# Kernel tuning notes

Measured on AMD Instinct MI355X. Metric: run time of the kernel, lower is better.

## Reference

```python
import jax, jax.numpy as jnp
import numpy as np

B, S, H = 2, 2048, 2048
NH, NKV, HD = 16, 4, 128
THETA = 10000.0


def _rope_cos_sin(seq_len, head_dim, theta, dtype):
    inv_freq = 1.0 / (theta ** (jnp.arange(0, head_dim, 2, dtype=jnp.float32) / head_dim))
    t = jnp.arange(seq_len, dtype=jnp.float32)
    freqs = t[:, None] * inv_freq[None, :]          # [S, HD/2]
    emb = jnp.concatenate([freqs, freqs], axis=-1)  # [S, HD]
    return jnp.cos(emb).astype(dtype), jnp.sin(emb).astype(dtype)


def _rotate_half(x):
    d = x.shape[-1] // 2
    return jnp.concatenate([-x[..., d:], x[..., :d]], axis=-1)


def setup_inputs() -> dict:
    key = jax.random.key(0)
    ks = jax.random.split(key, 5)
    x = jax.random.normal(ks[0], (B, S, H), dtype=jnp.float32)
    Wq = jax.random.normal(ks[1], (NH * HD, H), dtype=jnp.float32) * 0.02
    Wk = jax.random.normal(ks[2], (NKV * HD, H), dtype=jnp.float32) * 0.02
    Wv = jax.random.normal(ks[3], (NKV * HD, H), dtype=jnp.float32) * 0.02
    Wo = jax.random.normal(ks[4], (H, H), dtype=jnp.float32) * 0.02
    causal = jnp.tril(jnp.ones((S, S), dtype=bool))
    attention_mask = jnp.where(causal, 0.0, -1e9).astype(jnp.float32)[None, None]  # [1,1,S,S]
    return {"x": x, "attention_mask": attention_mask, "Wq": Wq, "Wk": Wk, "Wv": Wv, "Wo": Wo}


def reference(x, attention_mask, Wq, Wk, Wv, Wo):
    b, s, _ = x.shape
    q = (x @ Wq.T).reshape(b, s, NH, HD).transpose(0, 2, 1, 3)    # [b,nh,s,hd]
    k = (x @ Wk.T).reshape(b, s, NKV, HD).transpose(0, 2, 1, 3)   # [b,nkv,s,hd]
    v = (x @ Wv.T).reshape(b, s, NKV, HD).transpose(0, 2, 1, 3)
    cos, sin = _rope_cos_sin(s, HD, THETA, x.dtype)               # [s,hd] each
    cos = cos[None, None]; sin = sin[None, None]
    q = q * cos + _rotate_half(q) * sin
    k = k * cos + _rotate_half(k) * sin
    rep = NH // NKV
    k = jnp.repeat(k, rep, axis=1)                                 # [b,nh,s,hd]
    v = jnp.repeat(v, rep, axis=1)
    scores = jnp.einsum('bhqd,bhkd->bhqk', q, k) / jnp.sqrt(jnp.asarray(HD, x.dtype))
    scores = scores + attention_mask
    attn = jax.nn.softmax(scores, axis=-1)
    out = jnp.einsum('bhqk,bhkd->bhqd', attn, v)                   # [b,nh,s,hd]
    out = out.transpose(0, 2, 1, 3).reshape(b, s, NH * HD)
    return out @ Wo.T
```

## Files before the change

kernel.cpp:

```cpp
#include <hip/hip_runtime.h>

typedef unsigned short u16;
typedef __bf16 bf16x8 __attribute__((ext_vector_type(8)));
typedef float f32x4 __attribute__((ext_vector_type(4)));
typedef short s16x4 __attribute__((ext_vector_type(4)));

#define S_LEN  2048
#define NHEADS 16
#define NKVH   4
#define HDIM   128
#define BB     2
#define MROWS  4096
#define QKV_N  3072
#define HID    2048

__device__ __forceinline__ u16 f2b(float f) {
  union { float f; unsigned u; } x; x.f = f;
  unsigned r = x.u + 0x7fffu + ((x.u >> 16) & 1u);
  return (u16)(r >> 16);
}
__device__ __forceinline__ float b2f(u16 v) {
  union { unsigned u; float f; } x; x.u = ((unsigned)v) << 16;
  return x.f;
}
__device__ __forceinline__ void gload_lds16(const u16* g, u16* l) {
  __builtin_amdgcn_global_load_lds((__attribute__((address_space(1))) void*)g,
                                   (__attribute__((address_space(3))) void*)l,
                                   16, 0, 0);
}
__device__ __forceinline__ unsigned cvtpk(float lo, float hi) {
  unsigned r;
  asm("v_cvt_pk_bf16_f32 %0, %1, %2" : "=v"(r) : "v"(lo), "v"(hi));
  return r;
}
#if __has_builtin(__builtin_amdgcn_mfma_f32_16x16x16bf16_1k)
__device__ __forceinline__ f32x4 mfma16(s16x4 a, s16x4 b, f32x4 c) {
  return __builtin_amdgcn_mfma_f32_16x16x16bf16_1k(a, b, c, 0, 0, 0);
}
#else
__device__ __forceinline__ f32x4 mfma16(s16x4 a, s16x4 b, f32x4 c) {
  asm("v_mfma_f32_16x16x16_bf16 %0, %1, %2, %0" : "+v"(c) : "v"(a), "v"(b));
  return c;
}
#endif

#define SBAR() do { __builtin_amdgcn_sched_barrier(0); \
                    __builtin_amdgcn_s_barrier();      \
                    __builtin_amdgcn_sched_barrier(0); } while (0)

#define PB_X   8192
#define PB_WQ  (PB_X + 4096)
#define PB_WK  (PB_WQ + 1024)
#define PB_WV  (PB_WK + 1024)
#define PB_WO  (PB_WV + 4096)
#define PB_CS  (PB_WO + 512)
__global__ void k_prep(const float* __restrict__ x,
                       const float* __restrict__ Wq, const float* __restrict__ Wk,
                       const float* __restrict__ Wv, const float* __restrict__ Wo,
                       u16* __restrict__ xb, u16* __restrict__ Wqkvb,
                       u16* __restrict__ Wob, float* __restrict__ cs)
{
  const int bid = blockIdx.x, tid = threadIdx.x;
  const float* src; u16* dst; int i;
  if (bid < PB_X)       { i = bid * 256 + tid;            src = x;  dst = xb; }
  else if (bid < PB_WQ) { i = (bid - PB_X) * 256 + tid;   src = Wq; dst = Wqkvb; }
  else if (bid < PB_WK) { i = (bid - PB_WQ) * 256 + tid;  src = Wk; dst = Wqkvb + (size_t)2048 * HID; }
  else if (bid < PB_WV) { i = (bid - PB_WK) * 256 + tid;  src = Wv; dst = Wqkvb + (size_t)2560 * HID; }
  else if (bid < PB_WO) { i = (bid - PB_WV) * 256 + tid;  src = Wo; dst = Wob; }
  else {
    const int p = (bid - PB_WO) * 256 + tid;
    const int s = p >> 6, j = p & 63;
    float inv = expf(-(float)j * 0.14391156831212787f);
    float ang = (float)s * inv;
    float c, sn; sincosf(ang, &sn, &c);
    cs[p * 2 + 0] = c; cs[p * 2 + 1] = sn;
    return;
  }
  float4 v = ((const float4*)src)[i];
  ushort4 o;
  o.x = f2b(v.x); o.y = f2b(v.y); o.z = f2b(v.z); o.w = f2b(v.w);
  ((ushort4*)dst)[i] = o;
}

#define MFMA_GRP(AV, BV, MO, NO)                                              \
  __builtin_amdgcn_s_setprio(1);                                              \
  _Pragma("unroll") for (int kk = 0; kk < 2; ++kk)                            \
  _Pragma("unroll") for (int mm = 0; mm < 4; ++mm)                            \
  _Pragma("unroll") for (int nn = 0; nn < 2; ++nn)                            \
    acc[(MO) + mm][(NO) + nn] = __builtin_amdgcn_mfma_f32_16x16x32_bf16(      \
        AV[kk][mm], BV[kk][nn], acc[(MO) + mm][(NO) + nn], 0, 0, 0);          \
  __builtin_amdgcn_s_setprio(0);

template <int OUT_BF16>
__global__ __launch_bounds__(512, 2) void k_gemm256(
    const u16* __restrict__ A, const u16* __restrict__ Bm, void* __restrict__ Cv,
    int M, int N, int K)
{
  __shared__ u16 AL[2][2][8192];
  __shared__ u16 BL[2][2][8192];
  const int tid = threadIdx.x;
  const int wave = tid >> 6, lane = tid & 63;
  const int l15 = lane & 15, l4 = lane >> 4;
  const int wr = wave >> 2, wc = wave & 3;
  const int gx = gridDim.x;
  const int nwg = gx * gridDim.y;
  int bid = blockIdx.y * gx + blockIdx.x;
  bid = (bid & 7) * (nwg >> 3) + (bid >> 3);
  const int col0 = (bid % gx) * 256, row0 = (bid / gx) * 256;

  int srcOff[2], dstD[2];
#pragma unroll
  for (int li = 0; li < 2; ++li) {
    const int D = (li * 512 + tid) * 16;
    const int off_p = D & 1023, si = D >> 10;
    const int off_l = off_p ^ (((off_p >> 9) & 1) << 5);
    const int R = si >> 1, C = si & 1;
    const int row = R * 16 + (off_l >> 6);
    const int colb = C * 64 + (off_l & 63);
    srcOff[li] = row * K + (colb >> 1);
    dstD[li] = D;
  }
  const int laneoff = (l15 * 64 + l4 * 16) ^ ((l15 >> 3) << 5);

  auto stage = [&](const u16* __restrict__ G, int grow0, int kb, u16* lds) {
#pragma unroll
    for (int li = 0; li < 2; ++li)
      gload_lds16(G + (size_t)grow0 * K + kb + srcOff[li],
                  (u16*)((char*)lds + dstD[li]));
  };

  f32x4 acc[8][4];
#pragma unroll
  for (int m = 0; m < 8; ++m)
#pragma unroll
    for (int n = 0; n < 4; ++n) acc[m][n] = f32x4{0.f, 0.f, 0.f, 0.f};

  const int nk = K >> 6;
  stage(A,  row0,       0,  &AL[0][0][0]);
  stage(A,  row0 + 128, 0,  &AL[0][1][0]);
  stage(Bm, col0,       0,  &BL[0][0][0]);
  stage(Bm, col0 + 128, 0,  &BL[0][1][0]);
  stage(A,  row0,       64, &AL[1][0][0]);
  stage(A,  row0 + 128, 64, &AL[1][1][0]);
  asm volatile("s_waitcnt vmcnt(4)" ::: "memory");
  SBAR();

  for (int t = 0; t < nk; ++t) {
    const int bi = t & 1;
    const bool sB = (t + 1 < nk);
    const bool sA = (t + 2 < nk);
    const char* Ab = (const char*)&AL[bi][wr][0];
    const char* Bb = (const char*)&BL[bi][wc >> 1][0] + (wc & 1) * 8192;
    bf16x8 a0[2][4], a1[2][4], b0[2][2], b1[2][2];
#pragma unroll
    for (int kk = 0; kk < 2; ++kk)
#pragma unroll
      for (int m = 0; m < 4; ++m)
        a0[kk][m] = *(const bf16x8*)(Ab + m * 2048 + kk * 1024 + laneoff);
#pragma unroll
    for (int kk = 0; kk < 2; ++kk)
#pragma unroll
      for (int n = 0; n < 2; ++n)
        b0[kk][n] = *(const bf16x8*)(Bb + n * 2048 + kk * 1024 + laneoff);
    if (sB) stage(Bm, col0, (t + 1) * 64, &BL[bi ^ 1][0][0]);
    SBAR();
    MFMA_GRP(a0, b0, 0, 0);
    SBAR();
#pragma unroll
    for (int kk = 0; kk < 2; ++kk)
#pragma unroll
      for (int m = 0; m < 4; ++m)
        a1[kk][m] = *(const bf16x8*)(Ab + (m + 4) * 2048 + kk * 1024 + laneoff);
    if (sB) stage(Bm, col0 + 128, (t + 1) * 64, &BL[bi ^ 1][1][0]);
    SBAR();
    MFMA_GRP(a1, b0, 4, 0);
    SBAR();
#pragma unroll
    for (int kk = 0; kk < 2; ++kk)
#pragma unroll
      for (int n = 0; n < 2; ++n)
        b1[kk][n] = *(const bf16x8*)(Bb + (n + 2) * 2048 + kk * 1024 + laneoff);
    if (sA) stage(A, row0, (t + 2) * 64, &AL[bi][0][0]);
    SBAR();
    MFMA_GRP(a1, b1, 4, 2);
    SBAR();
    if (sA) {
      stage(A, row0 + 128, (t + 2) * 64, &AL[bi][1][0]);
      asm volatile("s_waitcnt vmcnt(4)" ::: "memory");
    } else if (sB) {
      asm volatile("s_waitcnt vmcnt(0)" ::: "memory");
    }
    SBAR();
    MFMA_GRP(a0, b1, 0, 2);
    SBAR();
  }

#pragma unroll
  for (int m = 0; m < 8; ++m) {
    const int r = row0 + wr * 128 + m * 16 + l4 * 4;
#pragma unroll
    for (int n = 0; n < 4; ++n) {
      const int c = col0 + wc * 64 + n * 16 + l15;
#pragma unroll
      for (int j = 0; j < 4; ++j) {
        const float v = acc[m][n][j];
        if (OUT_BF16) ((u16*)Cv)[(size_t)(r + j) * N + c] = f2b(v);
        else          ((float*)Cv)[(size_t)(r + j) * N + c] = v;
      }
    }
  }
}

template <int OUT_BF16>
__global__ __launch_bounds__(256) void k_gemm_bt(
    const u16* __restrict__ A, const u16* __restrict__ Bm, void* __restrict__ Cv,
    int M, int N, int K)
{
  __shared__ u16 Al[2][128 * 32];
  __shared__ u16 Bl[2][128 * 32];
  const int tid = threadIdx.x;
  const int wave = tid >> 6, lane = tid & 63;
  const int l15 = lane & 15, l4 = lane >> 4;
  const int wr = wave >> 1, wc = wave & 1;
  const int row0 = blockIdx.y * 128, col0 = blockIdx.x * 128;

  f32x4 zero = {0.f, 0.f, 0.f, 0.f};
  f32x4 acc[4][4];
#pragma unroll
  for (int m = 0; m < 4; ++m)
#pragma unroll
    for (int n = 0; n < 4; ++n) acc[m][n] = zero;

  const int e0 = lane * 8;
  auto stage = [&](int buf, int kb) {
#pragma unroll
    for (int it = 0; it < 2; ++it) {
      const int chunk = it * 4 + wave;
      const int e = chunk * 512 + e0;
      const int r = e >> 5, c = e & 31;
      gload_lds16(A + (size_t)(row0 + r) * K + kb + c, &Al[buf][chunk * 512]);
      gload_lds16(Bm + (size_t)(col0 + r) * K + kb + c, &Bl[buf][chunk * 512]);
    }
  };

  stage(0, 0);
  asm volatile("s_waitcnt vmcnt(0)" ::: "memory");
  SBAR();
  int cur = 0;
  for (int kb = 0; kb < K; kb += 32) {
    if (kb + 32 < K) stage(cur ^ 1, kb + 32);
    bf16x8 af[4], bfv[4];
#pragma unroll
    for (int m = 0; m < 4; ++m)
      af[m] = *(const bf16x8*)(&Al[cur][(wr * 64 + m * 16 + l15) * 32 + l4 * 8]);
#pragma unroll
    for (int n = 0; n < 4; ++n)
      bfv[n] = *(const bf16x8*)(&Bl[cur][(wc * 64 + n * 16 + l15) * 32 + l4 * 8]);
    __builtin_amdgcn_s_setprio(1);
#pragma unroll
    for (int m = 0; m < 4; ++m)
#pragma unroll
      for (int n = 0; n < 4; ++n)
        acc[m][n] = __builtin_amdgcn_mfma_f32_16x16x32_bf16(af[m], bfv[n], acc[m][n], 0, 0, 0);
    __builtin_amdgcn_s_setprio(0);
    asm volatile("s_waitcnt vmcnt(0)" ::: "memory");
    SBAR();
    cur ^= 1;
  }
#pragma unroll
  for (int m = 0; m < 4; ++m) {
    const int r = row0 + wr * 64 + m * 16 + l4 * 4;
#pragma unroll
    for (int n = 0; n < 4; ++n) {
      const int c = col0 + wc * 64 + n * 16 + l15;
#pragma unroll
      for (int j = 0; j < 4; ++j) {
        const float v = acc[m][n][j];
        if (OUT_BF16) ((u16*)Cv)[(size_t)(r + j) * N + c] = f2b(v);
        else          ((float*)Cv)[(size_t)(r + j) * N + c] = v;
      }
    }
  }
}

__global__ __launch_bounds__(256) void k_ropev(
    const u16* __restrict__ qkv, const float* __restrict__ cs,
    u16* __restrict__ Qr, u16* __restrict__ Kr, u16* __restrict__ Vt)
{
  const int blk = blockIdx.x;
  const int b = blk >> 8, s0 = (blk & 255) << 3;
  const int tid = threadIdx.x;
  const float S2 = 0.08838834764831845f * 1.4426950408889634f;
#pragma unroll
  for (int p = tid; p < 1024; p += 256) {
    const int s = p >> 7, rem = p & 127, h = rem >> 3, j8 = (rem & 7) * 8;
    const int sg = s0 + s;
    const u16* src = qkv + (size_t)(b * S_LEN + sg) * QKV_N + h * 128 + j8;
    union { uint4 v; u16 u[8]; } lo, hi, olo, ohi;
    lo.v = *(const uint4*)(src);
    hi.v = *(const uint4*)(src + 64);
    const float* cp = cs + (size_t)(sg * 64 + j8) * 2;
#pragma unroll
    for (int k = 0; k < 8; ++k) {
      const float c = cp[k * 2], sn = cp[k * 2 + 1];
      const float x0 = b2f(lo.u[k]), x1 = b2f(hi.u[k]);
      olo.u[k] = f2b((x0 * c - x1 * sn) * S2);
      ohi.u[k] = f2b((x1 * c + x0 * sn) * S2);
    }
    u16* dst = Qr + ((size_t)(b * NHEADS + h) * S_LEN + sg) * HDIM + j8;
    *(uint4*)(dst) = olo.v;
    *(uint4*)(dst + 64) = ohi.v;
  }
  {
    const int p = tid;
    const int s = p >> 5, rem = p & 31, h = rem >> 3, j8 = (rem & 7) * 8;
    const int sg = s0 + s;
    const u16* src = qkv + (size_t)(b * S_LEN + sg) * QKV_N + 2048 + h * 128 + j8;
    union { uint4 v; u16 u[8]; } lo, hi, olo, ohi;
    lo.v = *(const uint4*)(src);
    hi.v = *(const uint4*)(src + 64);
    const float* cp = cs + (size_t)(sg * 64 + j8) * 2;
#pragma unroll
    for (int k = 0; k < 8; ++k) {
      const float c = cp[k * 2], sn = cp[k * 2 + 1];
      const float x0 = b2f(lo.u[k]), x1 = b2f(hi.u[k]);
      olo.u[k] = f2b(x0 * c - x1 * sn);
      ohi.u[k] = f2b(x1 * c + x0 * sn);
    }
    u16* dst = Kr + ((size_t)(b * NKVH + h) * S_LEN + sg) * HDIM + j8;
    *(uint4*)(dst) = olo.v;
    *(uint4*)(dst + 64) = ohi.v;
  }
#pragma unroll
  for (int vi = 0; vi < 2; ++vi) {
    const int idx = vi * 256 + tid, h = idx >> 7, d = idx & 127;
    union { u16 u[8]; uint4 v; } bb;
#pragma unroll
    for (int s = 0; s < 8; ++s)
      bb.u[s] = qkv[(size_t)(b * S_LEN + s0 + s) * QKV_N + 2560 + idx];
    *(uint4*)(Vt + ((size_t)(b * NKVH + h) * HDIM + d) * S_LEN + s0) = bb.v;
  }
}

__device__ __forceinline__ void attn_qtile(
    int qt, int lastPhase,
    const u16* __restrict__ Q, const u16* __restrict__ Kg, const u16* __restrict__ Vg,
    u16* __restrict__ Out, int bh,
    u16* Kl0, u16* Kl1, u16* Vl0, u16* Vl1,
    const int (&ko)[4], const int (&vo)[4],
    int wave, int lane, int& cur)
{
  const int l15 = lane & 15, l4 = lane >> 4;
  const int b = bh >> 4, h = bh & 15;
  const int qw0 = qt * 64 + wave * 16;
  const u16* Qg = Q + ((size_t)bh * S_LEN + qw0) * HDIM;

  bf16x8 qf[4];
#pragma unroll
  for (int kc = 0; kc < 4; ++kc)
    qf[kc] = *(const bf16x8*)(Qg + l15 * HDIM + kc * 32 + l4 * 8);

  f32x4 zero = {0.f, 0.f, 0.f, 0.f};
  f32x4 oacc[8];
#pragma unroll
  for (int i = 0; i < 8; ++i) oacc[i] = zero;
  float m_r = -1e30f, l_p = 0.f;

  const int nt = qt + 1;
  const int qg = qw0 + l15;

  for (int t = 0; t < nt; ++t) {
    const int kt = t * 64;
    u16* Vb = cur ? Vl1 : Vl0;
#pragma unroll
    for (int it = 0; it < 4; ++it)
      gload_lds16(Vg + (size_t)vo[it] + kt, Vb + (it * 4 + wave) * 512);
    const int hasNext = (t + 1 < nt) || (!lastPhase);
    const int ktn = (t + 1 < nt) ? kt + 64 : 0;
    u16* Kn = cur ? Kl0 : Kl1;
    if (hasNext) {
#pragma unroll
      for (int it = 0; it < 4; ++it)
        gload_lds16(Kg + (size_t)ktn * HDIM + ko[it], Kn + (it * 4 + wave) * 512);
      asm volatile("s_waitcnt vmcnt(8)" ::: "memory");
    } else {
      asm volatile("s_waitcnt vmcnt(4)" ::: "memory");
    }
    __builtin_amdgcn_sched_barrier(0);
    __builtin_amdgcn_s_barrier();
    __builtin_amdgcn_sched_barrier(0);

    const char* Kb = (const char*)(cur ? Kl1 : Kl0);
    f32x4 s[4];
#pragma unroll
    for (int n = 0; n < 4; ++n) s[n] = zero;
    __builtin_amdgcn_s_setprio(1);
#pragma unroll
    for (int n = 0; n < 4; ++n) {
      const int row = n * 16 + l15;
#pragma unroll
      for (int kc = 0; kc < 4; ++kc) {
        const int ab = (row * 256 + kc * 64 + l4 * 16) ^ ((row & 7) << 4);
        bf16x8 kf = *(const bf16x8*)(Kb + ab);
        s[n] = __builtin_amdgcn_mfma_f32_16x16x32_bf16(kf, qf[kc], s[n], 0, 0, 0);
      }
    }
    __builtin_amdgcn_s_setprio(0);
    float sv[4][4];
    if (kt + 63 > qw0) {
#pragma unroll
      for (int n = 0; n < 4; ++n)
#pragma unroll
        for (int j = 0; j < 4; ++j) {
          float x = s[n][j];
          if (kt + n * 16 + l4 * 4 + j > qg) x = -1e30f;
          sv[n][j] = x;
        }
    } else {
#pragma unroll
      for (int n = 0; n < 4; ++n)
#pragma unroll
        for (int j = 0; j < 4; ++j) sv[n][j] = s[n][j];
    }
    float pm = sv[0][0];
#pragma unroll
    for (int n = 0; n < 4; ++n)
#pragma unroll
      for (int j = 0; j < 4; ++j) pm = fmaxf(pm, sv[n][j]);
    if (!__all(pm <= m_r + 11.5416f)) {
      float pf = fmaxf(pm, __shfl_xor(pm, 16, 64));
      pf = fmaxf(pf, __shfl_xor(pf, 32, 64));
      const float mn = fmaxf(m_r, pf);
      const float sc = exp2f(m_r - mn);
      m_r = mn;
      l_p *= sc;
      float scq[4];
#pragma unroll
      for (int j = 0; j < 4; ++j) scq[j] = __shfl(sc, l4 * 4 + j, 64);
#pragma unroll
      for (int nd = 0; nd < 8; ++nd)
#pragma unroll
        for (int j = 0; j < 4; ++j) oacc[nd][j] *= scq[j];
    }
    union { unsigned u[2]; s16x4 v; } a[4];
#pragma unroll
    for (int n = 0; n < 4; ++n) {
      const float p0 = exp2f(sv[n][0] - m_r);
      const float p1 = exp2f(sv[n][1] - m_r);
      const float p2 = exp2f(sv[n][2] - m_r);
      const float p3 = exp2f(sv[n][3] - m_r);
      l_p += (p0 + p1) + (p2 + p3);
      a[n].u[0] = cvtpk(p0, p1);
      a[n].u[1] = cvtpk(p2, p3);
    }
    if (hasNext) asm volatile("s_waitcnt vmcnt(4)" ::: "memory");
    else         asm volatile("s_waitcnt vmcnt(0)" ::: "memory");
    __builtin_amdgcn_sched_barrier(0);
    __builtin_amdgcn_s_barrier();
    __builtin_amdgcn_sched_barrier(0);
    __builtin_amdgcn_s_setprio(1);
#pragma unroll
    for (int nd = 0; nd < 8; ++nd) {
      const int d = nd * 16 + l15;
      const int rowb = d * 128, swz = (d & 7) << 4;
#pragma unroll
      for (int n = 0; n < 4; ++n) {
        const int ab = (rowb + n * 32 + l4 * 8) ^ swz;
        s16x4 vf = *(const s16x4*)((const char*)Vb + ab);
        oacc[nd] = mfma16(a[n].v, vf, oacc[nd]);
      }
    }
    __builtin_amdgcn_s_setprio(0);
    cur ^= 1;
  }

  l_p += __shfl_xor(l_p, 16, 64);
  l_p += __shfl_xor(l_p, 32, 64);
  float il[4];
#pragma unroll
  for (int j = 0; j < 4; ++j) il[j] = 1.f / __shfl(l_p, l4 * 4 + j, 64);
  const size_t obase = ((size_t)b * S_LEN + qw0 + l4 * 4) * HID + h * HDIM;
#pragma unroll
  for (int nd = 0; nd < 8; ++nd)
#pragma unroll
    for (int j = 0; j < 4; ++j)
      Out[obase + (size_t)j * HID + nd * 16 + l15] = f2b(oacc[nd][j] * il[j]);
}

__global__ __launch_bounds__(256) void k_attn(
    const u16* __restrict__ Q, const u16* __restrict__ Kr,
    const u16* __restrict__ Vt, u16* __restrict__ Out)
{
  __shared__ u16 Kl[2][64 * 128];
  __shared__ u16 Vl[2][128 * 64];
  const int tid = threadIdx.x;
  const int wave = tid >> 6, lane = tid & 63;
  const int bh = blockIdx.x;
  const int pairi = blockIdx.y;
  const int b = bh >> 4, h = bh & 15;
  const int kvh = h >> 2;

  const u16* Kg = Kr + (size_t)(b * NKVH + kvh) * S_LEN * HDIM;
  const u16* Vg = Vt + (size_t)(b * NKVH + kvh) * HDIM * S_LEN;

  int ko[4], vo[4];
#pragma unroll
  for (int it = 0; it < 4; ++it) {
    const int c = it * 4 + wave;
    const int L = c * 1024 + lane * 16;
    const int r = L >> 8;  const int w2 = (L & 255) ^ ((r & 7) << 4);
    ko[it] = r * HDIM + (w2 >> 1);
    const int d = L >> 7;  const int wv = (L & 127) ^ ((d & 7) << 4);
    vo[it] = d * S_LEN + (wv >> 1);
  }
#pragma unroll
  for (int it = 0; it < 4; ++it)
    gload_lds16(Kg + ko[it], &Kl[0][(it * 4 + wave) * 512]);

  int cur = 0;
  attn_qtile(31 - pairi, 0, Q, Kg, Vg, Out, bh, &Kl[0][0], &Kl[1][0],
             &Vl[0][0], &Vl[1][0], ko, vo, wave, lane, cur);
  attn_qtile(pairi,      1, Q, Kg, Vg, Out, bh, &Kl[0][0], &Kl[1][0],
             &Vl[0][0], &Vl[1][0], ko, vo, wave, lane, cur);
}

extern "C" void kernel_launch(void* const* d_in, const int* in_sizes, int n_in,
                              void* d_out, int out_size, void* d_ws, size_t ws_size,
                              hipStream_t stream)
{
  const float* x  = (const float*)d_in[0];
  const float* Wq = (const float*)d_in[2];
  const float* Wk = (const float*)d_in[3];
  const float* Wv = (const float*)d_in[4];
  const float* Wo = (const float*)d_in[5];
  float* out = (float*)d_out;

  u16* xb    = (u16*)d_ws;
  u16* Wqkvb = xb    + (size_t)MROWS * HID;
  u16* Wob   = Wqkvb + (size_t)QKV_N * HID;
  u16* qkv   = Wob   + (size_t)HID * HID;
  u16* Qr    = qkv   + (size_t)MROWS * QKV_N;
  u16* Kr    = Qr    + (size_t)BB * NHEADS * S_LEN * HDIM;
  u16* Vt    = Kr    + (size_t)BB * NKVH * S_LEN * HDIM;
  u16* attn  = Vt    + (size_t)BB * NKVH * S_LEN * HDIM;
  float* cs  = (float*)(attn + (size_t)MROWS * HID);

  k_prep<<<dim3(PB_CS), 256, 0, stream>>>(x, Wq, Wk, Wv, Wo, xb, Wqkvb, Wob, cs);
  k_gemm256<1><<<dim3(QKV_N / 256, MROWS / 256), 512, 0, stream>>>(xb, Wqkvb, qkv, MROWS, QKV_N, HID);
  k_ropev<<<dim3(BB * 256), 256, 0, stream>>>(qkv, cs, Qr, Kr, Vt);
  k_attn<<<dim3(BB * NHEADS, 16), 256, 0, stream>>>(Qr, Kr, Vt, attn);
  k_gemm_bt<0><<<dim3(HID / 128, MROWS / 128), 256, 0, stream>>>(attn, Wob, out, MROWS, HID, HID);
}
```

Baseline: 208.6 us.

## Split attention into one q-tile per block with 32-wide KV tiles; use 256 GEMM for output

The attention kernel now assigns one 64-row query tile to each block (32 blocks per head) instead of pairing two tiles per block. It steps over keys in 32-wide tiles with halved LDS buffers and a matching V swizzle layout. The output projection switches from the 128-tile GEMM to the existing 256-tile GEMM kernel. The aim is more parallelism and occupancy in attention and better reuse in the final GEMM, at the cost of more loop iterations, extra barriers and a less balanced causal workload across blocks.

```diff
diff --git a/kernel.cpp b/kernel.cpp
--- a/kernel.cpp
+++ b/kernel.cpp
@@ -211,78 +211,6 @@
   }
 }
 
-template <int OUT_BF16>
-__global__ __launch_bounds__(256) void k_gemm_bt(
-    const u16* __restrict__ A, const u16* __restrict__ Bm, void* __restrict__ Cv,
-    int M, int N, int K)
-{
-  __shared__ u16 Al[2][128 * 32];
-  __shared__ u16 Bl[2][128 * 32];
-  const int tid = threadIdx.x;
-  const int wave = tid >> 6, lane = tid & 63;
-  const int l15 = lane & 15, l4 = lane >> 4;
-  const int wr = wave >> 1, wc = wave & 1;
-  const int row0 = blockIdx.y * 128, col0 = blockIdx.x * 128;
-
-  f32x4 zero = {0.f, 0.f, 0.f, 0.f};
-  f32x4 acc[4][4];
-#pragma unroll
-  for (int m = 0; m < 4; ++m)
-#pragma unroll
-    for (int n = 0; n < 4; ++n) acc[m][n] = zero;
-
-  const int e0 = lane * 8;
-  auto stage = [&](int buf, int kb) {
-#pragma unroll
-    for (int it = 0; it < 2; ++it) {
-      const int chunk = it * 4 + wave;
-      const int e = chunk * 512 + e0;
-      const int r = e >> 5, c = e & 31;
-      gload_lds16(A + (size_t)(row0 + r) * K + kb + c, &Al[buf][chunk * 512]);
-      gload_lds16(Bm + (size_t)(col0 + r) * K + kb + c, &Bl[buf][chunk * 512]);
-    }
-  };
-
-  stage(0, 0);
-  asm volatile("s_waitcnt vmcnt(0)" ::: "memory");
-  SBAR();
-  int cur = 0;
-  for (int kb = 0; kb < K; kb += 32) {
-    if (kb + 32 < K) stage(cur ^ 1, kb + 32);
-    bf16x8 af[4], bfv[4];
-#pragma unroll
-    for (int m = 0; m < 4; ++m)
-      af[m] = *(const bf16x8*)(&Al[cur][(wr * 64 + m * 16 + l15) * 32 + l4 * 8]);
-#pragma unroll
-    for (int n = 0; n < 4; ++n)
-      bfv[n] = *(const bf16x8*)(&Bl[cur][(wc * 64 + n * 16 + l15) * 32 + l4 * 8]);
-    __builtin_amdgcn_s_setprio(1);
-#pragma unroll
-    for (int m = 0; m < 4; ++m)
-#pragma unroll
-      for (int n = 0; n < 4; ++n)
-        acc[m][n] = __builtin_amdgcn_mfma_f32_16x16x32_bf16(af[m], bfv[n], acc[m][n], 0, 0, 0);
-    __builtin_amdgcn_s_setprio(0);
-    asm volatile("s_waitcnt vmcnt(0)" ::: "memory");
-    SBAR();
-    cur ^= 1;
-  }
-#pragma unroll
-  for (int m = 0; m < 4; ++m) {
-    const int r = row0 + wr * 64 + m * 16 + l4 * 4;
-#pragma unroll
-    for (int n = 0; n < 4; ++n) {
-      const int c = col0 + wc * 64 + n * 16 + l15;
-#pragma unroll
-      for (int j = 0; j < 4; ++j) {
-        const float v = acc[m][n][j];
-        if (OUT_BF16) ((u16*)Cv)[(size_t)(r + j) * N + c] = f2b(v);
-        else          ((float*)Cv)[(size_t)(r + j) * N + c] = v;
-      }
-    }
-  }
-}
-
 __global__ __launch_bounds__(256) void k_ropev(
     const u16* __restrict__ qkv, const float* __restrict__ cs,
     u16* __restrict__ Qr, u16* __restrict__ Kr, u16* __restrict__ Vt)
@@ -342,18 +270,41 @@
   }
 }
 
-__device__ __forceinline__ void attn_qtile(
-    int qt, int lastPhase,
-    const u16* __restrict__ Q, const u16* __restrict__ Kg, const u16* __restrict__ Vg,
-    u16* __restrict__ Out, int bh,
-    u16* Kl0, u16* Kl1, u16* Vl0, u16* Vl1,
-    const int (&ko)[4], const int (&vo)[4],
-    int wave, int lane, int& cur)
+__global__ __launch_bounds__(256) void k_attn(
+    const u16* __restrict__ Q, const u16* __restrict__ Kr,
+    const u16* __restrict__ Vt, u16* __restrict__ Out)
 {
+  __shared__ u16 Kl[2][32 * 128];
+  __shared__ u16 Vl[2][64 * 64];
+  const int tid = threadIdx.x;
+  const int wave = tid >> 6, lane = tid & 63;
   const int l15 = lane & 15, l4 = lane >> 4;
+  const int bh = blockIdx.x;
+  const int by = blockIdx.y;
   const int b = bh >> 4, h = bh & 15;
+  const int kvh = h >> 2;
+  const int aa = by & 7, kk_ = by >> 3;
+  const int qt = (kk_ == 0) ? aa : (kk_ == 1) ? 15 - aa : (kk_ == 2) ? 16 + aa : 31 - aa;
+
+  const u16* Kg = Kr + (size_t)(b * NKVH + kvh) * S_LEN * HDIM;
+  const u16* Vg = Vt + (size_t)(b * NKVH + kvh) * HDIM * S_LEN;
+
+  int ko[2], vo[2];
+#pragma unroll
+  for (int it = 0; it < 2; ++it) {
+    const int c = it * 4 + wave;
+    const int L = c * 1024 + lane * 16;
+    const int r = L >> 8;
+    const int w2 = (L & 255) ^ ((r & 7) << 4);
+    ko[it] = r * HDIM + (w2 >> 1);
+    const int row = L >> 7;
+    const int wv = (L & 127) ^ ((row & 7) << 4);
+    const int d = row * 2 + (wv >> 6);
+    vo[it] = d * S_LEN + ((wv & 63) >> 1);
+  }
+
   const int qw0 = qt * 64 + wave * 16;
-  const u16* Qg = Q + ((size_t)bh * S_LEN + qw0) * HDIM;
+  const u16* Qg = Q + ((size_t)(b * NHEADS + h) * S_LEN + qw0) * HDIM;
 
   bf16x8 qf[4];
 #pragma unroll
@@ -366,37 +317,38 @@
   for (int i = 0; i < 8; ++i) oacc[i] = zero;
   float m_r = -1e30f, l_p = 0.f;
 
-  const int nt = qt + 1;
+  const int nt = 2 * qt + 2;
   const int qg = qw0 + l15;
+  int cur = 0;
+
+#pragma unroll
+  for (int it = 0; it < 2; ++it)
+    gload_lds16(Kg + ko[it], &Kl[0][(it * 4 + wave) * 512]);
 
   for (int t = 0; t < nt; ++t) {
-    const int kt = t * 64;
-    u16* Vb = cur ? Vl1 : Vl0;
-#pragma unroll
-    for (int it = 0; it < 4; ++it)
+    const int kt = t * 32;
+    u16* Vb = cur ? &Vl[1][0] : &Vl[0][0];
+#pragma unroll
+    for (int it = 0; it < 2; ++it)
       gload_lds16(Vg + (size_t)vo[it] + kt, Vb + (it * 4 + wave) * 512);
-    const int hasNext = (t + 1 < nt) || (!lastPhase);
-    const int ktn = (t + 1 < nt) ? kt + 64 : 0;
-    u16* Kn = cur ? Kl0 : Kl1;
+    const int hasNext = (t + 1 < nt);
     if (hasNext) {
-#pragma unroll
-      for (int it = 0; it < 4; ++it)
-        gload_lds16(Kg + (size_t)ktn * HDIM + ko[it], Kn + (it * 4 + wave) * 512);
-      asm volatile("s_waitcnt vmcnt(8)" ::: "memory");
+      u16* Kn = cur ? &Kl[0][0] : &Kl[1][0];
+#pragma unroll
+      for (int it = 0; it < 2; ++it)
+        gload_lds16(Kg + (size_t)(kt + 32) * HDIM + ko[it], Kn + (it * 4 + wave) * 512);
+      asm volatile("s_waitcnt vmcnt(4)" ::: "memory");
     } else {
-      asm volatile("s_waitcnt vmcnt(4)" ::: "memory");
-    }
-    __builtin_amdgcn_sched_barrier(0);
-    __builtin_amdgcn_s_barrier();
-    __builtin_amdgcn_sched_barrier(0);
-
-    const char* Kb = (const char*)(cur ? Kl1 : Kl0);
-    f32x4 s[4];
-#pragma unroll
-    for (int n = 0; n < 4; ++n) s[n] = zero;
+      asm volatile("s_waitcnt vmcnt(2)" ::: "memory");
+    }
+    SBAR();
+
+    const char* Kb = (const char*)(cur ? &Kl[1][0] : &Kl[0][0]);
+    f32x4 s[2];
+    s[0] = zero; s[1] = zero;
     __builtin_amdgcn_s_setprio(1);
 #pragma unroll
-    for (int n = 0; n < 4; ++n) {
+    for (int n = 0; n < 2; ++n) {
       const int row = n * 16 + l15;
 #pragma unroll
       for (int kc = 0; kc < 4; ++kc) {
@@ -406,27 +358,18 @@
       }
     }
     __builtin_amdgcn_s_setprio(0);
-    float sv[4][4];
-    if (kt + 63 > qw0) {
-#pragma unroll
-      for (int n = 0; n < 4; ++n)
-#pragma unroll
-        for (int j = 0; j < 4; ++j) {
-          float x = s[n][j];
-          if (kt + n * 16 + l4 * 4 + j > qg) x = -1e30f;
-          sv[n][j] = x;
-        }
-    } else {
-#pragma unroll
-      for (int n = 0; n < 4; ++n)
-#pragma unroll
-        for (int j = 0; j < 4; ++j) sv[n][j] = s[n][j];
-    }
-    float pm = sv[0][0];
-#pragma unroll
-    for (int n = 0; n < 4; ++n)
-#pragma unroll
-      for (int j = 0; j < 4; ++j) pm = fmaxf(pm, sv[n][j]);
+    if (kt + 31 > qw0) {
+#pragma unroll
+      for (int n = 0; n < 2; ++n)
+#pragma unroll
+        for (int j = 0; j < 4; ++j)
+          if (kt + n * 16 + l4 * 4 + j > qg) s[n][j] = -1e30f;
+    }
+    float pm = s[0][0];
+#pragma unroll
+    for (int n = 0; n < 2; ++n)
+#pragma unroll
+      for (int j = 0; j < 4; ++j) pm = fmaxf(pm, s[n][j]);
     if (!__all(pm <= m_r + 11.5416f)) {
       float pf = fmaxf(pm, __shfl_xor(pm, 16, 64));
       pf = fmaxf(pf, __shfl_xor(pf, 32, 64));
@@ -442,29 +385,28 @@
 #pragma unroll
         for (int j = 0; j < 4; ++j) oacc[nd][j] *= scq[j];
     }
-    union { unsigned u[2]; s16x4 v; } a[4];
-#pragma unroll
-    for (int n = 0; n < 4; ++n) {
-      const float p0 = exp2f(sv[n][0] - m_r);
-      const float p1 = exp2f(sv[n][1] - m_r);
-      const float p2 = exp2f(sv[n][2] - m_r);
-      const float p3 = exp2f(sv[n][3] - m_r);
+    union { unsigned u[2]; s16x4 v; } a[2];
+#pragma unroll
+    for (int n = 0; n < 2; ++n) {
+      const float p0 = exp2f(s[n][0] - m_r);
+      const float p1 = exp2f(s[n][1] - m_r);
+      const float p2 = exp2f(s[n][2] - m_r);
+      const float p3 = exp2f(s[n][3] - m_r);
       l_p += (p0 + p1) + (p2 + p3);
       a[n].u[0] = cvtpk(p0, p1);
       a[n].u[1] = cvtpk(p2, p3);
     }
-    if (hasNext) asm volatile("s_waitcnt vmcnt(4)" ::: "memory");
+    if (hasNext) asm volatile("s_waitcnt vmcnt(2)" ::: "memory");
     else         asm volatile("s_waitcnt vmcnt(0)" ::: "memory");
-    __builtin_amdgcn_sched_barrier(0);
-    __builtin_amdgcn_s_barrier();
-    __builtin_amdgcn_sched_barrier(0);
+    SBAR();
     __builtin_amdgcn_s_setprio(1);
 #pragma unroll
     for (int nd = 0; nd < 8; ++nd) {
       const int d = nd * 16 + l15;
-      const int rowb = d * 128, swz = (d & 7) << 4;
-#pragma unroll
-      for (int n = 0; n < 4; ++n) {
+      const int rowb = (d >> 1) * 128 + (d & 1) * 64;
+      const int swz = ((d >> 1) & 7) << 4;
+#pragma unroll
+      for (int n = 0; n < 2; ++n) {
         const int ab = (rowb + n * 32 + l4 * 8) ^ swz;
         s16x4 vf = *(const s16x4*)((const char*)Vb + ab);
         oacc[nd] = mfma16(a[n].v, vf, oacc[nd]);
@@ -485,43 +427,6 @@
 #pragma unroll
     for (int j = 0; j < 4; ++j)
       Out[obase + (size_t)j * HID + nd * 16 + l15] = f2b(oacc[nd][j] * il[j]);
-}
-
-__global__ __launch_bounds__(256) void k_attn(
-    const u16* __restrict__ Q, const u16* __restrict__ Kr,
-    const u16* __restrict__ Vt, u16* __restrict__ Out)
-{
-  __shared__ u16 Kl[2][64 * 128];
-  __shared__ u16 Vl[2][128 * 64];
-  const int tid = threadIdx.x;
-  const int wave = tid >> 6, lane = tid & 63;
-  const int bh = blockIdx.x;
-  const int pairi = blockIdx.y;
-  const int b = bh >> 4, h = bh & 15;
-  const int kvh = h >> 2;
-
-  const u16* Kg = Kr + (size_t)(b * NKVH + kvh) * S_LEN * HDIM;
-  const u16* Vg = Vt + (size_t)(b * NKVH + kvh) * HDIM * S_LEN;
-
-  int ko[4], vo[4];
-#pragma unroll
-  for (int it = 0; it < 4; ++it) {
-    const int c = it * 4 + wave;
-    const int L = c * 1024 + lane * 16;
-    const int r = L >> 8;  const int w2 = (L & 255) ^ ((r & 7) << 4);
-    ko[it] = r * HDIM + (w2 >> 1);
-    const int d = L >> 7;  const int wv = (L & 127) ^ ((d & 7) << 4);
-    vo[it] = d * S_LEN + (wv >> 1);
-  }
-#pragma unroll
-  for (int it = 0; it < 4; ++it)
-    gload_lds16(Kg + ko[it], &Kl[0][(it * 4 + wave) * 512]);
-
-  int cur = 0;
-  attn_qtile(31 - pairi, 0, Q, Kg, Vg, Out, bh, &Kl[0][0], &Kl[1][0],
-             &Vl[0][0], &Vl[1][0], ko, vo, wave, lane, cur);
-  attn_qtile(pairi,      1, Q, Kg, Vg, Out, bh, &Kl[0][0], &Kl[1][0],
-             &Vl[0][0], &Vl[1][0], ko, vo, wave, lane, cur);
 }
 
 extern "C" void kernel_launch(void* const* d_in, const int* in_sizes, int n_in,
@@ -548,6 +453,6 @@
   k_prep<<<dim3(PB_CS), 256, 0, stream>>>(x, Wq, Wk, Wv, Wo, xb, Wqkvb, Wob, cs);
   k_gemm256<1><<<dim3(QKV_N / 256, MROWS / 256), 512, 0, stream>>>(xb, Wqkvb, qkv, MROWS, QKV_N, HID);
   k_ropev<<<dim3(BB * 256), 256, 0, stream>>>(qkv, cs, Qr, Kr, Vt);
-  k_attn<<<dim3(BB * NHEADS, 16), 256, 0, stream>>>(Qr, Kr, Vt, attn);
-  k_gemm_bt<0><<<dim3(HID / 128, MROWS / 128), 256, 0, stream>>>(attn, Wob, out, MROWS, HID, HID);
-}
+  k_attn<<<dim3(BB * NHEADS, 32), 256, 0, stream>>>(Qr, Kr, Vt, attn);
+  k_gemm256<0><<<dim3(HID / 256, MROWS / 256), 512, 0, stream>>>(attn, Wob, out, MROWS, HID, HID);
+}
```

After: 226.9 us. 8.8% more time.

## Share K/V tiles across two GQA heads per attention block and swizzle GEMM blocks

Applied to the files above, without the earlier changes.

The attention kernel now runs 512 threads per block, with two query heads that share the same KV head, so each K/V tile staged in LDS serves twice as many waves. Each wave issues half as many global-to-LDS loads, and the grid shrinks from 32x16 to 16x16 blocks. The output-projection GEMM remaps block IDs into an XCD-aware order (bid&7 spreading) to improve L2 locality across chiplets. The cost is fewer, larger attention blocks, which may lower occupancy or load balance. The code also relies on an SBAR macro that is not defined in the shown portion.

```diff
diff --git a/kernel.cpp b/kernel.cpp
--- a/kernel.cpp
+++ b/kernel.cpp
@@ -222,7 +222,11 @@
   const int wave = tid >> 6, lane = tid & 63;
   const int l15 = lane & 15, l4 = lane >> 4;
   const int wr = wave >> 1, wc = wave & 1;
-  const int row0 = blockIdx.y * 128, col0 = blockIdx.x * 128;
+  const int gx = gridDim.x;
+  const int nwg = gx * gridDim.y;
+  int bid = blockIdx.y * gx + blockIdx.x;
+  bid = (bid & 7) * (nwg >> 3) + (bid >> 3);
+  const int row0 = (bid / gx) * 128, col0 = (bid % gx) * 128;
 
   f32x4 zero = {0.f, 0.f, 0.f, 0.f};
   f32x4 acc[4][4];
@@ -347,12 +351,12 @@
     const u16* __restrict__ Q, const u16* __restrict__ Kg, const u16* __restrict__ Vg,
     u16* __restrict__ Out, int bh,
     u16* Kl0, u16* Kl1, u16* Vl0, u16* Vl1,
-    const int (&ko)[4], const int (&vo)[4],
-    int wave, int lane, int& cur)
+    const int (&ko)[2], const int (&vo)[2],
+    int wave, int w4, int lane, int& cur)
 {
   const int l15 = lane & 15, l4 = lane >> 4;
   const int b = bh >> 4, h = bh & 15;
-  const int qw0 = qt * 64 + wave * 16;
+  const int qw0 = qt * 64 + w4 * 16;
   const u16* Qg = Q + ((size_t)bh * S_LEN + qw0) * HDIM;
 
   bf16x8 qf[4];
@@ -373,22 +377,20 @@
     const int kt = t * 64;
     u16* Vb = cur ? Vl1 : Vl0;
 #pragma unroll
-    for (int it = 0; it < 4; ++it)
-      gload_lds16(Vg + (size_t)vo[it] + kt, Vb + (it * 4 + wave) * 512);
+    for (int it = 0; it < 2; ++it)
+      gload_lds16(Vg + (size_t)vo[it] + kt, Vb + (it * 8 + wave) * 512);
     const int hasNext = (t + 1 < nt) || (!lastPhase);
     const int ktn = (t + 1 < nt) ? kt + 64 : 0;
     u16* Kn = cur ? Kl0 : Kl1;
     if (hasNext) {
 #pragma unroll
-      for (int it = 0; it < 4; ++it)
-        gload_lds16(Kg + (size_t)ktn * HDIM + ko[it], Kn + (it * 4 + wave) * 512);
-      asm volatile("s_waitcnt vmcnt(8)" ::: "memory");
+      for (int it = 0; it < 2; ++it)
+        gload_lds16(Kg + (size_t)ktn * HDIM + ko[it], Kn + (it * 8 + wave) * 512);
+      asm volatile("s_waitcnt vmcnt(4)" ::: "memory");
     } else {
-      asm volatile("s_waitcnt vmcnt(4)" ::: "memory");
-    }
-    __builtin_amdgcn_sched_barrier(0);
-    __builtin_amdgcn_s_barrier();
-    __builtin_amdgcn_sched_barrier(0);
+      asm volatile("s_waitcnt vmcnt(2)" ::: "memory");
+    }
+    SBAR();
 
     const char* Kb = (const char*)(cur ? Kl1 : Kl0);
     f32x4 s[4];
@@ -453,11 +455,9 @@
       a[n].u[0] = cvtpk(p0, p1);
       a[n].u[1] = cvtpk(p2, p3);
     }
-    if (hasNext) asm volatile("s_waitcnt vmcnt(4)" ::: "memory");
+    if (hasNext) asm volatile("s_waitcnt vmcnt(2)" ::: "memory");
     else         asm volatile("s_waitcnt vmcnt(0)" ::: "memory");
-    __builtin_amdgcn_sched_barrier(0);
-    __builtin_amdgcn_s_barrier();
-    __builtin_amdgcn_sched_barrier(0);
+    SBAR();
     __builtin_amdgcn_s_setprio(1);
 #pragma unroll
     for (int nd = 0; nd < 8; ++nd) {
@@ -487,7 +487,7 @@
       Out[obase + (size_t)j * HID + nd * 16 + l15] = f2b(oacc[nd][j] * il[j]);
 }
 
-__global__ __launch_bounds__(256) void k_attn(
+__global__ __launch_bounds__(512) void k_attn(
     const u16* __restrict__ Q, const u16* __restrict__ Kr,
     const u16* __restrict__ Vt, u16* __restrict__ Out)
 {
@@ -495,18 +495,20 @@
   __shared__ u16 Vl[2][128 * 64];
   const int tid = threadIdx.x;
   const int wave = tid >> 6, lane = tid & 63;
-  const int bh = blockIdx.x;
+  const int bx = blockIdx.x;
   const int pairi = blockIdx.y;
-  const int b = bh >> 4, h = bh & 15;
-  const int kvh = h >> 2;
+  const int kvh = bx & 3, b = (bx >> 2) & 1, hp = bx >> 3;
+  const int h = kvh * 4 + hp + (wave >> 2) * 2;
+  const int bh = b * NHEADS + h;
+  const int w4 = wave & 3;
 
   const u16* Kg = Kr + (size_t)(b * NKVH + kvh) * S_LEN * HDIM;
   const u16* Vg = Vt + (size_t)(b * NKVH + kvh) * HDIM * S_LEN;
 
-  int ko[4], vo[4];
-#pragma unroll
-  for (int it = 0; it < 4; ++it) {
-    const int c = it * 4 + wave;
+  int ko[2], vo[2];
+#pragma unroll
+  for (int it = 0; it < 2; ++it) {
+    const int c = it * 8 + wave;
     const int L = c * 1024 + lane * 16;
     const int r = L >> 8;  const int w2 = (L & 255) ^ ((r & 7) << 4);
     ko[it] = r * HDIM + (w2 >> 1);
@@ -514,14 +516,14 @@
     vo[it] = d * S_LEN + (wv >> 1);
   }
 #pragma unroll
-  for (int it = 0; it < 4; ++it)
-    gload_lds16(Kg + ko[it], &Kl[0][(it * 4 + wave) * 512]);
+  for (int it = 0; it < 2; ++it)
+    gload_lds16(Kg + ko[it], &Kl[0][(it * 8 + wave) * 512]);
 
   int cur = 0;
   attn_qtile(31 - pairi, 0, Q, Kg, Vg, Out, bh, &Kl[0][0], &Kl[1][0],
-             &Vl[0][0], &Vl[1][0], ko, vo, wave, lane, cur);
+             &Vl[0][0], &Vl[1][0], ko, vo, wave, w4, lane, cur);
   attn_qtile(pairi,      1, Q, Kg, Vg, Out, bh, &Kl[0][0], &Kl[1][0],
-             &Vl[0][0], &Vl[1][0], ko, vo, wave, lane, cur);
+             &Vl[0][0], &Vl[1][0], ko, vo, wave, w4, lane, cur);
 }
 
 extern "C" void kernel_launch(void* const* d_in, const int* in_sizes, int n_in,
@@ -548,6 +550,6 @@
   k_prep<<<dim3(PB_CS), 256, 0, stream>>>(x, Wq, Wk, Wv, Wo, xb, Wqkvb, Wob, cs);
   k_gemm256<1><<<dim3(QKV_N / 256, MROWS / 256), 512, 0, stream>>>(xb, Wqkvb, qkv, MROWS, QKV_N, HID);
   k_ropev<<<dim3(BB * 256), 256, 0, stream>>>(qkv, cs, Qr, Kr, Vt);
-  k_attn<<<dim3(BB * NHEADS, 16), 256, 0, stream>>>(Qr, Kr, Vt, attn);
+  k_attn<<<dim3(16, 16), 512, 0, stream>>>(Qr, Kr, Vt, attn);
   k_gemm_bt<0><<<dim3(HID / 128, MROWS / 128), 256, 0, stream>>>(attn, Wob, out, MROWS, HID, HID);
 }
```

New measurement: 209.8 us. No clear change (+0.6%).
